# Kernel optimization log

Hardware: AMD Instinct MI355X
Metric: run time of the kernel (lower is better)

Reference implementation:

```python
import jax, jax.numpy as jnp
import numpy as np

HEADS = 16
EPS = 1e-6


def _rms_norm(x, g):
    # RMSNorm computed in fp32 (matches torch x.float())
    xf = x.astype(jnp.float32)
    y = xf * jax.lax.rsqrt(jnp.mean(xf * xf, axis=-1, keepdims=True) + EPS)
    return y.astype(x.dtype) * g


def setup_inputs() -> dict:
    key = jax.random.key(0)
    ks = jax.random.split(key, 6)
    b, n, dim, emb_dim = 4, 2048, 2048, 2048
    d_head = dim // HEADS
    return {
        "x": jax.random.normal(ks[0], (b, n, dim), jnp.float32),
        "emb": jax.random.normal(ks[1], (b, 1, emb_dim), jnp.float32),
        "W_emb": jax.random.normal(ks[2], (emb_dim, 2 * dim), jnp.float32) * (emb_dim ** -0.5),
        "b_emb": jnp.zeros((2 * dim,), jnp.float32),
        "g_norm": jnp.ones((dim,), jnp.float32),
        "W_qkv": jax.random.normal(ks[3], (dim, 3 * dim), jnp.float32) * (dim ** -0.5),
        "g_q": jnp.ones((d_head,), jnp.float32),
        "g_k": jnp.ones((d_head,), jnp.float32),
        "W_out": jax.random.normal(ks[4], (dim, dim), jnp.float32) * (dim ** -0.5),
    }


def reference(x, emb, W_emb, b_emb, g_norm, W_qkv, g_q, g_k, W_out):
    b, n, dim = x.shape
    h = HEADS
    d = dim // h
    # AdaLN conditioning: RMSNorm(x) * (1 + scale) + shift
    scale_shift = emb @ W_emb + b_emb            # [b, 1, 2*dim]
    scale, shift = jnp.split(scale_shift, 2, axis=-1)
    xn = _rms_norm(x, g_norm) * (1.0 + scale) + shift
    # fused QKV projection then split to heads
    qkv = xn @ W_qkv                             # [b, n, 3*dim]
    qkv = qkv.reshape(b, n, 3, h, d)
    q, k, v = jnp.moveaxis(qkv, 2, 0)            # each [b, n, h, d]
    q = jnp.swapaxes(q, 1, 2)                    # [b, h, n, d]
    k = jnp.swapaxes(k, 1, 2)
    v = jnp.swapaxes(v, 1, 2)
    # per-head QK RMSNorm
    q = _rms_norm(q, g_q)
    k = _rms_norm(k, g_k)
    # SDPA (no mask, default scale 1/sqrt(d))
    logits = jnp.einsum("bhqd,bhkd->bhqk", q, k) * (d ** -0.5)
    attn = jax.nn.softmax(logits, axis=-1)
    o = jnp.einsum("bhqk,bhkd->bhqd", attn, v)   # [b, h, n, d]
    o = jnp.swapaxes(o, 1, 2).reshape(b, n, dim)
    return o + o @ W_out
```

## Files before the change

### kernel.cpp

```cpp
#include <hip/hip_runtime.h>
#include <stdint.h>

typedef unsigned short u16;
typedef __bf16 bf16x8 __attribute__((ext_vector_type(8)));
typedef float  f32x4  __attribute__((ext_vector_type(4)));
typedef unsigned short u16x4v __attribute__((ext_vector_type(4)));

#define HEADS 16
#define DIM   2048
#define DHEAD 128
#define SEQ   2048
#define QKVN  (3*DIM)

__device__ __forceinline__ float bf2f(u16 u){
  union { unsigned int i; float f; } c; c.i = ((unsigned int)u) << 16; return c.f;
}
__device__ __forceinline__ u16 f2bf(float f){
  union { float f; unsigned int i; } c; c.f = f;
  unsigned int r = c.i + 0x7fffu + ((c.i >> 16) & 1u);
  return (u16)(r >> 16);
}

__device__ __forceinline__ void gl_lds16(const u16* g, u16* l){
  __builtin_amdgcn_global_load_lds((const __attribute__((address_space(1))) void*)g,
                                   (__attribute__((address_space(3))) void*)l,
                                   16, 0, 0);
}

__global__ void k_probe(const u16* __restrict__ w, int* __restrict__ flag){
  int i = threadIdx.x;
  u16 u = w[(size_t)i*131072];
  float v = bf2f(u);
  float a = fabsf(v);
  int wild = (a >= 1e4f) || (a > 0.f && a < 1e-4f) || (v != v);
  #pragma unroll
  for (int off=1;off<64;off<<=1) wild += __shfl_xor(wild, off, 64);
  if (i==0) *flag = (wild >= 32) ? 1 : 0;
}

__global__ __launch_bounds__(256) void k_sentinel1000(u16* __restrict__ out){
  size_t base = ((size_t)blockIdx.x*256 + threadIdx.x)*8;
  uint4 w; w.x=w.y=w.z=w.w=0x447A447Au;
  *(uint4*)(out + base) = w;
}
__global__ __launch_bounds__(256) void k_sentinel500(const int* __restrict__ flag, u16* __restrict__ out){
  if (*flag) return;
  size_t base = ((size_t)blockIdx.x*256 + threadIdx.x)*8;
  uint4 w; w.x=w.y=w.z=w.w=0x43FA43FAu;
  *(uint4*)(out + base) = w;
}

__global__ __launch_bounds__(256) void k_transpose_f(const int* __restrict__ flag,
                                                     const float* __restrict__ src, u16* __restrict__ dst,
                                                     int R, int C){
  if (!*flag) return;
  __shared__ u16 t[64][65];
  int tid = threadIdx.x;
  int c0 = blockIdx.x*64, r0 = blockIdx.y*64;
  #pragma unroll
  for (int i=0;i<16;++i){
    int idx = tid + i*256; int r = idx>>6, c = idx&63;
    t[r][c] = f2bf(src[(size_t)(r0+r)*C + c0 + c]);
  }
  __syncthreads();
  #pragma unroll
  for (int i=0;i<16;++i){
    int idx = tid + i*256; int r = idx>>6, c = idx&63;
    dst[(size_t)(c0+r)*R + r0 + c] = t[c][r];
  }
}

__global__ __launch_bounds__(256) void k_scale_shift(const int* __restrict__ flag,
                                                     const float* __restrict__ emb, const float* __restrict__ W,
                                                     const float* __restrict__ bias, float* __restrict__ ss){
  if (!*flag) return;
  __shared__ float eL[4*2048];
  int tid = threadIdx.x;
  for (int i=tid;i<4*2048;i+=256) eL[i] = emb[i];
  __syncthreads();
  int col = blockIdx.x*256 + tid;
  float a0=0,a1=0,a2=0,a3=0;
  for (int k=0;k<2048;++k){
    float w = W[(size_t)k*4096 + col];
    a0 += eL[k]*w; a1 += eL[2048+k]*w; a2 += eL[4096+k]*w; a3 += eL[6144+k]*w;
  }
  float bb = bias[col];
  ss[col]=a0+bb; ss[4096+col]=a1+bb; ss[8192+col]=a2+bb; ss[12288+col]=a3+bb;
}

__global__ __launch_bounds__(256) void k_rmsnorm_mod(const int* __restrict__ flag,
                                                     const float* __restrict__ x, const float* __restrict__ ss,
                                                     const float* __restrict__ g, u16* __restrict__ xn){
  if (!*flag) return;
  int row = blockIdx.x, tid = threadIdx.x;
  int b = row >> 11;
  const float* xr = x + (size_t)row*DIM;
  float4 v0 = ((const float4*)xr)[tid*2];
  float4 v1 = ((const float4*)xr)[tid*2+1];
  float xf[8] = {v0.x,v0.y,v0.z,v0.w,v1.x,v1.y,v1.z,v1.w};
  float s = 0.f;
  #pragma unroll
  for (int j=0;j<8;++j) s += xf[j]*xf[j];
  #pragma unroll
  for (int off=1;off<64;off<<=1) s += __shfl_xor(s, off, 64);
  __shared__ float red[4];
  if ((tid&63)==0) red[tid>>6] = s;
  __syncthreads();
  float tot = red[0]+red[1]+red[2]+red[3];
  float rs = rsqrtf(tot*(1.f/2048.f) + 1e-6f);
  const float* sb = ss + b*4096;
  unsigned int o[4];
  #pragma unroll
  for (int j=0;j<4;++j){
    int c0 = tid*8 + j*2;
    float y0 = xf[j*2]  *rs*g[c0]   * (1.f + sb[c0])   + sb[2048+c0];
    float y1 = xf[j*2+1]*rs*g[c0+1] * (1.f + sb[c0+1]) + sb[2048+c0+1];
    o[j] = (unsigned int)f2bf(y0) | ((unsigned int)f2bf(y1)<<16);
  }
  uint4 ov; ov.x=o[0]; ov.y=o[1]; ov.z=o[2]; ov.w=o[3];
  *(uint4*)&xn[(size_t)row*DIM + tid*8] = ov;
}

__global__ __launch_bounds__(256) void k_qk_norm(const int* __restrict__ flag,
                                                 u16* __restrict__ qkv, const float* __restrict__ gq,
                                                 const float* __restrict__ gk){
  if (!*flag) return;
  int tid=threadIdx.x, lane=tid&63, wv=tid>>6;
  unsigned int gid = blockIdx.x*4 + wv;
  int s = (int)(gid >> 17);
  unsigned int rr = gid & 131071u;
  unsigned int bn = rr >> 4; int head = (int)(rr & 15u);
  u16* p = qkv + (size_t)bn*QKVN + s*DIM + head*DHEAD + lane*2;
  unsigned int vv = *(const unsigned int*)p;
  float e0 = bf2f((u16)(vv&0xffffu)), e1 = bf2f((u16)(vv>>16));
  float sum = e0*e0 + e1*e1;
  #pragma unroll
  for (int off=1;off<64;off<<=1) sum += __shfl_xor(sum, off, 64);
  float rs = rsqrtf(sum*(1.f/128.f) + 1e-6f);
  const float* g = s ? gk : gq;
  float g0 = g[lane*2], g1 = g[lane*2+1];
  unsigned int o0 = f2bf(e0*rs*g0), o1 = f2bf(e1*rs*g1);
  *(unsigned int*)p = o0 | (o1<<16);
}

__global__ __launch_bounds__(256) void k_gemm_bt(const int* __restrict__ flag,
                                                 const u16* __restrict__ A, const u16* __restrict__ Bt,
                                                 void* __restrict__ Cv, const u16* __restrict__ addsrc,
                                                 int M, int N, int K, int outf32){
  if (!*flag) return;
  __shared__ __align__(16) u16 As[128*64];
  __shared__ __align__(16) u16 Bs[128*64];
  int tid = threadIdx.x, lane = tid&63, wv = tid>>6;
  int l15 = lane&15, qd = lane>>4;
  int swz = l15&7;

  int gx = gridDim.x, gy = gridDim.y;
  int nwg = gx*gy;
  int lin = blockIdx.y*gx + blockIdx.x;
  int sid = (nwg & 7) ? lin : ((lin & 7)*(nwg>>3) + (lin>>3));
  int bx = sid % gx, by = sid / gx;

  int row0 = by*128, col0 = bx*128;
  int wm = (wv&1)*64, wn = (wv>>1)*64;
  f32x4 acc[4][4];
  #pragma unroll
  for (int mt=0;mt<4;++mt)
    #pragma unroll
    for (int nt=0;nt<4;++nt) acc[mt][nt] = (f32x4){0.f,0.f,0.f,0.f};

  int r8 = tid>>3;
  int s8 = tid&7;

  for (int k0=0;k0<K;k0+=64){
    #pragma unroll
    for (int i=0;i<4;++i){
      int r = i*32 + r8;
      int kslot = s8 ^ (r&7);
      gl_lds16(A  + (size_t)(row0 + r)*K + k0 + kslot*8, &As[i*2048 + wv*512]);
      gl_lds16(Bt + (size_t)(col0 + r)*K + k0 + kslot*8, &Bs[i*2048 + wv*512]);
    }
    __syncthreads();
    #pragma unroll
    for (int ks=0;ks<2;++ks){
      bf16x8 af[4], bfr[4];
      #pragma unroll
      for (int mt=0;mt<4;++mt)
        af[mt]  = *(const bf16x8*)&As[(wm+mt*16+l15)*64 + (((ks*4+qd) ^ swz)*8)];
      #pragma unroll
      for (int nt=0;nt<4;++nt)
        bfr[nt] = *(const bf16x8*)&Bs[(wn+nt*16+l15)*64 + (((ks*4+qd) ^ swz)*8)];
      #pragma unroll
      for (int mt=0;mt<4;++mt)
        #pragma unroll
        for (int nt=0;nt<4;++nt)
          acc[mt][nt] = __builtin_amdgcn_mfma_f32_16x16x32_bf16(af[mt], bfr[nt], acc[mt][nt], 0,0,0);
    }
    __syncthreads();
  }
  #pragma unroll
  for (int mt=0;mt<4;++mt)
    #pragma unroll
    for (int nt=0;nt<4;++nt)
      #pragma unroll
      for (int r=0;r<4;++r){
        int row = row0 + wm + mt*16 + qd*4 + r;
        int col = col0 + wn + nt*16 + l15;
        float v = acc[mt][nt][r];
        if (addsrc) v += bf2f(addsrc[(size_t)row*N + col]);
        if (outf32) ((float*)Cv)[(size_t)row*N + col] = v;
        else        ((u16*)Cv)[(size_t)row*N + col] = f2bf(v);
      }
}

__global__ __launch_bounds__(256) void k_vtrans(const int* __restrict__ flag,
                                                const u16* __restrict__ qkv, u16* __restrict__ Vt){
  if (!*flag) return;
  __shared__ u16 t[64][66];
  int tid = threadIdx.x;
  int n0 = blockIdx.x*64, d0 = blockIdx.y*64, bh = blockIdx.z;
  int b = bh>>4, h = bh&15;
  #pragma unroll
  for (int i=0;i<2;++i){
    int idx = tid + i*256;
    int r = idx>>3, c8 = (idx&7)*8;
    uint4 v = *(const uint4*)(qkv + (size_t)(b*SEQ + n0 + r)*QKVN + 2*DIM + h*DHEAD + d0 + c8);
    const u16* pv = (const u16*)&v;
    #pragma unroll
    for (int j=0;j<8;++j) t[r][c8+j] = pv[j];
  }
  __syncthreads();
  #pragma unroll
  for (int i=0;i<2;++i){
    int idx = tid + i*256;
    int dr = idx>>3, nc8 = (idx&7)*8;
    union { u16 s[8]; uint4 v; } u;
    #pragma unroll
    for (int j=0;j<8;++j) u.s[j] = t[nc8+j][dr];
    *(uint4*)(Vt + (size_t)(bh*DHEAD + d0 + dr)*SEQ + n0 + nc8) = u.v;
  }
}

#define KT 64
__global__ __launch_bounds__(256, 3) void k_attn_mfma(const int* __restrict__ flag,
                                                      const u16* __restrict__ qkv,
                                                      const u16* __restrict__ Vt,
                                                      u16* __restrict__ O){
  if (!*flag) return;
  __shared__ __align__(16) u16 Ks[KT*DHEAD];
  __shared__ __align__(16) u16 Vs[DHEAD*KT];
  __shared__ __align__(16) u16 Ps[4*32*KT];

  int tid = threadIdx.x;
  int w = tid>>6, lane = tid&63;
  int l15 = lane&15, qd = lane>>4;
  int swz = (l15&7)<<3;

  int bh = blockIdx.y; int b = bh>>4, h = bh&15;
  int q0 = blockIdx.x*128 + w*32;

  const u16* Qb = qkv + (size_t)(b*SEQ + q0 + l15)*QKVN + h*DHEAD;
  bf16x8 qf0[4], qf1[4];
  #pragma unroll
  for (int ks=0;ks<4;++ks){
    qf0[ks] = *(const bf16x8*)(Qb + ks*32 + qd*8);
    qf1[ks] = *(const bf16x8*)(Qb + (size_t)16*QKVN + ks*32 + qd*8);
  }

  f32x4 o0[8], o1[8];
  #pragma unroll
  for (int cf=0;cf<8;++cf){ o0[cf] = (f32x4){0.f,0.f,0.f,0.f}; o1[cf] = (f32x4){0.f,0.f,0.f,0.f}; }
  float mrun0=-3e38f, mrun1=-3e38f, lrun0=0.f, lrun1=0.f;
  const float sc = 0.08838834764831845f;

  const u16* Kb0 = qkv + (size_t)b*SEQ*QKVN + DIM + h*DHEAD;
  const u16* Vb0 = Vt + (size_t)bh*DHEAD*SEQ;
  u16* Pw = &Ps[w*32*KT];

  int rK0 = w*4 + (lane>>4), cK = lane&15;
  int rV0 = w*8 + (lane>>3), cV = lane&7;

  for (int kt0=0; kt0<SEQ; kt0+=KT){
    __syncthreads();
    #pragma unroll
    for (int i=0;i<4;++i){
      int rK = i*16 + rK0;
      gl_lds16(Kb0 + (size_t)(kt0 + rK)*QKVN + (cK ^ (rK&7))*8, &Ks[i*2048 + w*512]);
    }
    #pragma unroll
    for (int i=0;i<4;++i){
      int rV = i*32 + rV0;
      gl_lds16(Vb0 + (size_t)rV*SEQ + kt0 + (cV ^ (rV&7))*8, &Vs[i*2048 + w*512]);
    }
    __syncthreads();

    f32x4 s0[4], s1[4];
    #pragma unroll
    for (int rf=0;rf<4;++rf){ s0[rf] = (f32x4){0.f,0.f,0.f,0.f}; s1[rf] = (f32x4){0.f,0.f,0.f,0.f}; }
    __builtin_amdgcn_s_setprio(1);
    #pragma unroll
    for (int ks=0;ks<4;++ks){
      #pragma unroll
      for (int rf=0;rf<4;++rf){
        bf16x8 kb = *(const bf16x8*)&Ks[(rf*16+l15)*DHEAD + ((ks*32+qd*8) ^ swz)];
        s0[rf] = __builtin_amdgcn_mfma_f32_16x16x32_bf16(kb, qf0[ks], s0[rf], 0,0,0);
        s1[rf] = __builtin_amdgcn_mfma_f32_16x16x32_bf16(kb, qf1[ks], s1[rf], 0,0,0);
      }
    }
    __builtin_amdgcn_s_setprio(0);

    float pm0 = -3e38f, pm1 = -3e38f;
    #pragma unroll
    for (int rf=0;rf<4;++rf)
      #pragma unroll
      for (int r=0;r<4;++r){
        pm0 = fmaxf(pm0, s0[rf][r]);
        pm1 = fmaxf(pm1, s1[rf][r]);
      }
    pm0 = fmaxf(pm0, __shfl_xor(pm0, 16, 64)); pm0 = fmaxf(pm0, __shfl_xor(pm0, 32, 64));
    pm1 = fmaxf(pm1, __shfl_xor(pm1, 16, 64)); pm1 = fmaxf(pm1, __shfl_xor(pm1, 32, 64));
    pm0 *= sc; pm1 *= sc;

    int defer = __all(pm0 <= mrun0 + 8.f) & __all(pm1 <= mrun1 + 8.f);
    if (!defer){
      float mn0 = fmaxf(mrun0, pm0), mn1 = fmaxf(mrun1, pm1);
      float a0 = __expf(mrun0 - mn0), a1 = __expf(mrun1 - mn1);
      mrun0 = mn0; mrun1 = mn1;
      lrun0 *= a0; lrun1 *= a1;
      #pragma unroll
      for (int r=0;r<4;++r){
        int src = (lane & 48) | (qd*4 + r);
        float ar0 = __shfl(a0, src, 64);
        float ar1 = __shfl(a1, src, 64);
        #pragma unroll
        for (int cf=0;cf<8;++cf){ o0[cf][r] *= ar0; o1[cf][r] *= ar1; }
      }
    }

    float rsum0 = 0.f, rsum1 = 0.f;
    #pragma unroll
    for (int rf=0;rf<4;++rf){
      u16x4v pk0, pk1;
      #pragma unroll
      for (int r=0;r<4;++r){
        float e0 = __expf(s0[rf][r]*sc - mrun0); u16 pb0 = f2bf(e0); rsum0 += bf2f(pb0); pk0[r] = pb0;
        float e1 = __expf(s1[rf][r]*sc - mrun1); u16 pb1 = f2bf(e1); rsum1 += bf2f(pb1); pk1[r] = pb1;
      }
      int cb = (rf*16 + qd*4) ^ swz;
      *(u16x4v*)&Pw[l15*KT + cb]      = pk0;
      *(u16x4v*)&Pw[(16+l15)*KT + cb] = pk1;
    }
    rsum0 += __shfl_xor(rsum0, 16, 64); rsum0 += __shfl_xor(rsum0, 32, 64);
    rsum1 += __shfl_xor(rsum1, 16, 64); rsum1 += __shfl_xor(rsum1, 32, 64);
    lrun0 += rsum0; lrun1 += rsum1;

    bf16x8 pf0[2], pf1[2];
    #pragma unroll
    for (int ks=0;ks<2;++ks){
      pf0[ks] = *(const bf16x8*)&Pw[l15*KT + ((ks*32+qd*8) ^ swz)];
      pf1[ks] = *(const bf16x8*)&Pw[(16+l15)*KT + ((ks*32+qd*8) ^ swz)];
    }
    __builtin_amdgcn_s_setprio(1);
    #pragma unroll
    for (int ks=0;ks<2;++ks){
      #pragma unroll
      for (int cf=0;cf<8;++cf){
        bf16x8 vb = *(const bf16x8*)&Vs[(cf*16+l15)*KT + ((ks*32+qd*8) ^ swz)];
        o0[cf] = __builtin_amdgcn_mfma_f32_16x16x32_bf16(pf0[ks], vb, o0[cf], 0,0,0);
        o1[cf] = __builtin_amdgcn_mfma_f32_16x16x32_bf16(pf1[ks], vb, o1[cf], 0,0,0);
      }
    }
    __builtin_amdgcn_s_setprio(0);
  }

  float iv0 = 1.f / lrun0, iv1 = 1.f / lrun1;
  #pragma unroll
  for (int r=0;r<4;++r){
    int src = (lane & 48) | (qd*4 + r);
    float a0 = __shfl(iv0, src, 64);
    float a1 = __shfl(iv1, src, 64);
    int row0 = q0 + qd*4 + r;
    u16* O0 = O + (size_t)(b*SEQ + row0)*DIM + h*DHEAD;
    u16* O1 = O + (size_t)(b*SEQ + row0 + 16)*DIM + h*DHEAD;
    #pragma unroll
    for (int cf=0;cf<8;++cf){
      O0[cf*16 + l15] = f2bf(o0[cf][r] * a0);
      O1[cf*16 + l15] = f2bf(o1[cf][r] * a1);
    }
  }
}

extern "C" void kernel_launch(void* const* d_in, const int* in_sizes, int n_in,
                              void* d_out, int out_size, void* d_ws, size_t ws_size,
                              hipStream_t stream){
  const float* x      = (const float*)d_in[0];
  const float* emb    = (const float*)d_in[1];
  const float* W_emb  = (const float*)d_in[2];
  const float* b_emb  = (const float*)d_in[3];
  const float* g_norm = (const float*)d_in[4];
  const float* W_qkv  = (const float*)d_in[5];
  const float* g_q    = (const float*)d_in[6];
  const float* g_k    = (const float*)d_in[7];
  const float* W_out  = (const float*)d_in[8];

  const size_t REQUIRED = 167837952;
  if (ws_size < REQUIRED){
    k_sentinel1000<<<dim3(8192), dim3(256), 0, stream>>>((u16*)d_out);
    return;
  }

  char* ws = (char*)d_ws;
  size_t off = 0;
  int*   flag = (int*)(ws + off);  off += 256;
  float* ss   = (float*)(ws + off); off += (size_t)4*4096*4;
  u16* qkv    = (u16*)(ws + off);   off += (size_t)8192*6144*2;
  u16* WqkvT  = (u16*)(ws + off);   off += (size_t)6144*2048*2;
  u16* WoutT  = (u16*)(ws + off);   off += (size_t)2048*2048*2;
  u16* xn     = (u16*)(ws + off);   off += (size_t)8192*2048*2;
  u16* o_buf  = xn;
  u16* Vt     = (u16*)d_out;

  dim3 blk(256);
  k_probe      <<<dim3(1), dim3(64), 0, stream>>>((const u16*)d_in[5], flag);
  k_transpose_f<<<dim3(96,32),  blk, 0, stream>>>(flag, W_qkv, WqkvT, 2048, 6144);
  k_transpose_f<<<dim3(32,32),  blk, 0, stream>>>(flag, W_out, WoutT, 2048, 2048);
  k_scale_shift<<<dim3(16),     blk, 0, stream>>>(flag, emb, W_emb, b_emb, ss);
  k_rmsnorm_mod<<<dim3(8192),   blk, 0, stream>>>(flag, x, ss, g_norm, xn);
  k_gemm_bt    <<<dim3(48,64),  blk, 0, stream>>>(flag, xn, WqkvT, qkv, nullptr, 8192, 6144, 2048, 0);
  k_qk_norm    <<<dim3(65536),  blk, 0, stream>>>(flag, qkv, g_q, g_k);
  k_vtrans     <<<dim3(32,2,64),blk, 0, stream>>>(flag, qkv, Vt);
  k_attn_mfma  <<<dim3(16,64),  blk, 0, stream>>>(flag, qkv, Vt, o_buf);
  k_gemm_bt    <<<dim3(16,64),  blk, 0, stream>>>(flag, o_buf, WoutT, d_out, o_buf, 8192, 2048, 2048, 1);
  k_sentinel500<<<dim3(8192),   blk, 0, stream>>>(flag, (u16*)d_out);
}
```

Measured before the change: 1.007 ms.

## Use 256x256 GEMM tiles with double-buffered LDS prefetch

Rewrites the bf16 GEMM kernel to compute 256x256 tiles with 512 threads (8 waves, each 128x64). It double-buffers A/B in LDS so the next K-slice loads asynchronously while MFMAs consume the current one, waiting with s_waitcnt vmcnt(8) plus raw barriers and raising wave priority during the MFMA block. This targets global-load latency and per-tile reuse in both projection GEMMs. It raises LDS use to 128KB and accumulator registers to 128 floats, which may cut occupancy. The output GEMM grid drops to 256 blocks, which may underfill the GPU.

After: 949.1 us. 1.06x faster.

```diff
diff --git a/kernel.cpp b/kernel.cpp
--- a/kernel.cpp
+++ b/kernel.cpp
@@ -143,13 +143,13 @@
   *(unsigned int*)p = o0 | (o1<<16);
 }
 
-__global__ __launch_bounds__(256) void k_gemm_bt(const int* __restrict__ flag,
-                                                 const u16* __restrict__ A, const u16* __restrict__ Bt,
-                                                 void* __restrict__ Cv, const u16* __restrict__ addsrc,
-                                                 int M, int N, int K, int outf32){
-  if (!*flag) return;
-  __shared__ __align__(16) u16 As[128*64];
-  __shared__ __align__(16) u16 Bs[128*64];
+__global__ __launch_bounds__(512, 2) void k_gemm_bt(const int* __restrict__ flag,
+                                                    const u16* __restrict__ A, const u16* __restrict__ Bt,
+                                                    void* __restrict__ Cv, const u16* __restrict__ addsrc,
+                                                    int M, int N, int K, int outf32){
+  if (!*flag) return;
+  __shared__ __align__(16) u16 As[2][256*64];
+  __shared__ __align__(16) u16 Bs[2][256*64];
   int tid = threadIdx.x, lane = tid&63, wv = tid>>6;
   int l15 = lane&15, qd = lane>>4;
   int swz = l15&7;
@@ -160,52 +160,74 @@
   int sid = (nwg & 7) ? lin : ((lin & 7)*(nwg>>3) + (lin>>3));
   int bx = sid % gx, by = sid / gx;
 
-  int row0 = by*128, col0 = bx*128;
-  int wm = (wv&1)*64, wn = (wv>>1)*64;
-  f32x4 acc[4][4];
-  #pragma unroll
-  for (int mt=0;mt<4;++mt)
-    #pragma unroll
-    for (int nt=0;nt<4;++nt) acc[mt][nt] = (f32x4){0.f,0.f,0.f,0.f};
-
-  int r8 = tid>>3;
-  int s8 = tid&7;
-
-  for (int k0=0;k0<K;k0+=64){
+  int row0 = by*256, col0 = bx*256;
+  int wr = wv>>2, wc = wv&3;
+  int wm = wr*128, wn = wc*64;
+
+  f32x4 acc[8][4];
+  #pragma unroll
+  for (int mt=0;mt<8;++mt)
+    #pragma unroll
+    for (int nt2=0;nt2<4;++nt2) acc[mt][nt2] = (f32x4){0.f,0.f,0.f,0.f};
+
+  int rs_ = wv*8 + (lane>>3);
+  int cs_ = lane&7;
+  int ntk = K>>6;
+
+  #pragma unroll
+  for (int i=0;i<4;++i){
+    int r = i*64 + rs_;
+    int c = cs_ ^ (r&7);
+    gl_lds16(A  + (size_t)(row0+r)*K + c*8, &As[0][i*4096 + wv*512]);
+    gl_lds16(Bt + (size_t)(col0+r)*K + c*8, &Bs[0][i*4096 + wv*512]);
+  }
+  asm volatile("s_waitcnt vmcnt(0)" ::: "memory");
+  __builtin_amdgcn_s_barrier();
+
+  for (int t=0; t<ntk; ++t){
+    int cur = t&1, nxt = cur^1;
+    int ts = (t+1 < ntk) ? t+1 : t;
+    int k0 = ts*64;
     #pragma unroll
     for (int i=0;i<4;++i){
-      int r = i*32 + r8;
-      int kslot = s8 ^ (r&7);
-      gl_lds16(A  + (size_t)(row0 + r)*K + k0 + kslot*8, &As[i*2048 + wv*512]);
-      gl_lds16(Bt + (size_t)(col0 + r)*K + k0 + kslot*8, &Bs[i*2048 + wv*512]);
-    }
-    __syncthreads();
+      int r = i*64 + rs_;
+      int c = cs_ ^ (r&7);
+      gl_lds16(A  + (size_t)(row0+r)*K + k0 + c*8, &As[nxt][i*4096 + wv*512]);
+      gl_lds16(Bt + (size_t)(col0+r)*K + k0 + c*8, &Bs[nxt][i*4096 + wv*512]);
+    }
+    asm volatile("s_waitcnt vmcnt(8)" ::: "memory");
+    __builtin_amdgcn_s_barrier();
+
+    __builtin_amdgcn_s_setprio(1);
     #pragma unroll
     for (int ks=0;ks<2;++ks){
-      bf16x8 af[4], bfr[4];
-      #pragma unroll
-      for (int mt=0;mt<4;++mt)
-        af[mt]  = *(const bf16x8*)&As[(wm+mt*16+l15)*64 + (((ks*4+qd) ^ swz)*8)];
-      #pragma unroll
-      for (int nt=0;nt<4;++nt)
-        bfr[nt] = *(const bf16x8*)&Bs[(wn+nt*16+l15)*64 + (((ks*4+qd) ^ swz)*8)];
-      #pragma unroll
-      for (int mt=0;mt<4;++mt)
+      bf16x8 af[8], bfr[4];
+      #pragma unroll
+      for (int mt=0;mt<8;++mt)
+        af[mt]  = *(const bf16x8*)&As[cur][(wm+mt*16+l15)*64 + (((ks*4+qd) ^ swz)*8)];
+      #pragma unroll
+      for (int nt2=0;nt2<4;++nt2)
+        bfr[nt2] = *(const bf16x8*)&Bs[cur][(wn+nt2*16+l15)*64 + (((ks*4+qd) ^ swz)*8)];
+      #pragma unroll
+      for (int mt=0;mt<8;++mt)
         #pragma unroll
-        for (int nt=0;nt<4;++nt)
-          acc[mt][nt] = __builtin_amdgcn_mfma_f32_16x16x32_bf16(af[mt], bfr[nt], acc[mt][nt], 0,0,0);
-    }
-    __syncthreads();
-  }
-  #pragma unroll
-  for (int mt=0;mt<4;++mt)
-    #pragma unroll
-    for (int nt=0;nt<4;++nt)
+        for (int nt2=0;nt2<4;++nt2)
+          acc[mt][nt2] = __builtin_amdgcn_mfma_f32_16x16x32_bf16(af[mt], bfr[nt2], acc[mt][nt2], 0,0,0);
+    }
+    __builtin_amdgcn_s_setprio(0);
+    __builtin_amdgcn_sched_barrier(0);
+    __builtin_amdgcn_s_barrier();
+  }
+
+  #pragma unroll
+  for (int mt=0;mt<8;++mt)
+    #pragma unroll
+    for (int nt2=0;nt2<4;++nt2)
       #pragma unroll
       for (int r=0;r<4;++r){
         int row = row0 + wm + mt*16 + qd*4 + r;
-        int col = col0 + wn + nt*16 + l15;
-        float v = acc[mt][nt][r];
+        int col = col0 + wn + nt2*16 + l15;
+        float v = acc[mt][nt2][r];
         if (addsrc) v += bf2f(addsrc[(size_t)row*N + col]);
         if (outf32) ((float*)Cv)[(size_t)row*N + col] = v;
         else        ((u16*)Cv)[(size_t)row*N + col] = f2bf(v);
@@ -419,16 +441,16 @@
   u16* o_buf  = xn;
   u16* Vt     = (u16*)d_out;
 
-  dim3 blk(256);
+  dim3 blk(256), blk512(512);
   k_probe      <<<dim3(1), dim3(64), 0, stream>>>((const u16*)d_in[5], flag);
   k_transpose_f<<<dim3(96,32),  blk, 0, stream>>>(flag, W_qkv, WqkvT, 2048, 6144);
   k_transpose_f<<<dim3(32,32),  blk, 0, stream>>>(flag, W_out, WoutT, 2048, 2048);
   k_scale_shift<<<dim3(16),     blk, 0, stream>>>(flag, emb, W_emb, b_emb, ss);
   k_rmsnorm_mod<<<dim3(8192),   blk, 0, stream>>>(flag, x, ss, g_norm, xn);
-  k_gemm_bt    <<<dim3(48,64),  blk, 0, stream>>>(flag, xn, WqkvT, qkv, nullptr, 8192, 6144, 2048, 0);
+  k_gemm_bt    <<<dim3(24,32),  blk512, 0, stream>>>(flag, xn, WqkvT, qkv, nullptr, 8192, 6144, 2048, 0);
   k_qk_norm    <<<dim3(65536),  blk, 0, stream>>>(flag, qkv, g_q, g_k);
   k_vtrans     <<<dim3(32,2,64),blk, 0, stream>>>(flag, qkv, Vt);
   k_attn_mfma  <<<dim3(16,64),  blk, 0, stream>>>(flag, qkv, Vt, o_buf);
-  k_gemm_bt    <<<dim3(16,64),  blk, 0, stream>>>(flag, o_buf, WoutT, d_out, o_buf, 8192, 2048, 2048, 1);
+  k_gemm_bt    <<<dim3(8,32),   blk512, 0, stream>>>(flag, o_buf, WoutT, d_out, o_buf, 8192, 2048, 2048, 1);
   k_sentinel500<<<dim3(8192),   blk, 0, stream>>>(flag, (u16*)d_out);
 }
```
